# Kernel optimization log

Measured on AMD Instinct MI355X. Metric: run time of the kernel, lower is better.

Reference implementation:

```python
import jax, jax.numpy as jnp
import numpy as np

B, N, E, H = 2, 2048, 512, 8
D = E // H
SCALE_BASE = 512.0
EPS = 1e-6


def _xpos_tables(n, d):
    # XPOS (torchscale): per-dim scale ramp + standard sinusoidal freqs
    half = d // 2
    xscale = (np.arange(0, d, 2, dtype=np.float32) + 0.4 * d) / (1.4 * d)  # [half]
    min_pos = -(n // 2)
    power = (np.arange(min_pos, n + min_pos, dtype=np.float32) / SCALE_BASE)[:, None]
    scale = xscale[None, :] ** power                                       # [n, half]
    inv_freq = 1.0 / (10000.0 ** (np.arange(0, half, dtype=np.float32) / half))
    sinusoid = np.arange(n, dtype=np.float32)[:, None] * inv_freq[None, :]  # [n, half]
    return (jnp.asarray(np.sin(sinusoid), jnp.float32),
            jnp.asarray(np.cos(sinusoid), jnp.float32),
            jnp.asarray(scale, jnp.float32))


def _dup_interleave(m):
    # [n, half] -> [n, d], each column repeated twice interleaved
    return jnp.repeat(m, 2, axis=-1)


def _rotate_every_two(x):
    x1, x2 = x[..., ::2], x[..., 1::2]
    return jnp.stack((-x2, x1), axis=-1).reshape(x.shape)


def _apply_xpos(x, sin, cos, scale):
    s = _dup_interleave(sin * scale)  # [n, d]
    c = _dup_interleave(cos * scale)
    return x * c + _rotate_every_two(x) * s


def _decay_mask(n, dtype=jnp.float32):
    # gammas per head: 1 - exp(linspace(log(1/32), log(1/512), H))
    gammas = 1.0 - jnp.exp(jnp.linspace(np.log(1.0 / 32), np.log(1.0 / 512), H)).astype(dtype)
    pos = jnp.arange(n, dtype=dtype)
    dist = pos[:, None] - pos[None, :]                 # [n, s]
    dist_c = jnp.where(dist >= 0, dist, 0.0)
    return jnp.where(dist[None] >= 0, gammas[:, None, None] ** dist_c[None], 0.0)  # [h, n, s]


def _msr_forward(query, key, value, Wq, bq, Wk, bk, Wv, bv, Wg, bg, Wo, bo):
    b, n, e = query.shape
    q = (query @ Wq.T + bq).reshape(b, n, H, D).transpose(0, 2, 1, 3)  # [b,h,n,d]
    k = (key   @ Wk.T + bk).reshape(b, n, H, D).transpose(0, 2, 1, 3)
    v = (value @ Wv.T + bv).reshape(b, n, H, D).transpose(0, 2, 1, 3)

    sin, cos, scale = _xpos_tables(n, D)
    q = _apply_xpos(q, sin, cos, scale)
    k = _apply_xpos(k, sin, cos, 1.0 / scale)  # downscale=True

    k = k / jnp.asarray(np.sqrt(D), q.dtype)   # scale = head_dim ** 0.5
    mask = _decay_mask(n, q.dtype)             # [h,n,s]

    sim = jnp.einsum('bhnd,bhsd->bhns', q, k) * mask[None]
    ret = jnp.einsum('bhns,bhsd->bhnd', sim, v)  # [b,h,n,d]

    # GroupNorm(groups=H, channels=H, affine=False) on [(b n), h, d]:
    # normalize each (b, n, h) slice over its d elements
    mean = ret.mean(axis=-1, keepdims=True)
    var = ret.var(axis=-1, keepdims=True)
    ret = (ret - mean) / jnp.sqrt(var + EPS)

    ret = ret.transpose(0, 2, 1, 3).reshape(b, n, e)
    gate = jax.nn.silu(query @ Wg.T + bg)
    return (ret * gate) @ Wo.T + bo


def setup_inputs() -> dict:
    key = jax.random.key(0)
    ks = jax.random.split(key, 13)
    std = float(np.sqrt(2.0 / (E + E)))  # xavier_normal for square Linear
    mk = lambda k: jax.random.normal(k, (E, E), jnp.float32) * std
    return {
        'query': jax.random.normal(ks[0], (B, N, E), jnp.float32),
        'key':   jax.random.normal(ks[1], (B, N, E), jnp.float32),
        'value': jax.random.normal(ks[2], (B, N, E), jnp.float32),
        'Wq': mk(ks[3]), 'bq': jnp.zeros((E,), jnp.float32),
        'Wk': mk(ks[4]), 'bk': jnp.zeros((E,), jnp.float32),
        'Wv': mk(ks[5]), 'bv': jnp.zeros((E,), jnp.float32),
        'Wg': mk(ks[6]), 'bg': jnp.zeros((E,), jnp.float32),
        'Wo': mk(ks[7]), 'bo': jnp.zeros((E,), jnp.float32),
    }


def reference(query, key, value, Wq, bq, Wk, bk, Wv, bv, Wg, bg, Wo, bo):
    return _msr_forward(query, key, value, Wq, bq, Wk, bk, Wv, bv, Wg, bg, Wo, bo)
```

## Files before the change

kernel.cpp:

```cpp
#include <hip/hip_runtime.h>
#include <math.h>

#define Bc 2
#define Nc 2048
#define Ec 512
#define Hc 8
#define Dc 64
#define Mc 4096
#define NT 32
#define Cc 64

typedef short bf16x8 __attribute__((ext_vector_type(8)));
typedef float f32x4 __attribute__((ext_vector_type(4)));

#define GLOAD(g, l) __builtin_amdgcn_global_load_lds(                        \
    (const __attribute__((address_space(1))) unsigned*)(const void*)(g),     \
    (__attribute__((address_space(3))) unsigned*)(void*)(l), 16, 0, 0)

__device__ __forceinline__ unsigned short f2bf(float x) {
    union { float f; unsigned u; } v; v.f = x;
    unsigned r = v.u + 0x7fffu + ((v.u >> 16) & 1u);
    return (unsigned short)(r >> 16);
}
__device__ __forceinline__ float bf2f(unsigned short b) {
    union { float f; unsigned u; } v; v.u = ((unsigned)b) << 16;
    return v.f;
}

__device__ __forceinline__ float get_gamma(int h) {
    const float l0 = -3.4657359028f;
    const float l1 = -6.2383246250f;
    return 1.0f - expf(l0 + (l1 - l0) * ((float)h / 7.0f));
}

struct SplitArgs {
    const float* src[8];
    unsigned short* hi[8];
    unsigned short* lo[8];
    int n[8];
};

__global__ __launch_bounds__(256) void prep_kernel(SplitArgs a,
                                                   float* __restrict__ sinS,
                                                   float* __restrict__ cosS,
                                                   float* __restrict__ sinIS,
                                                   float* __restrict__ cosIS) {
    int y = blockIdx.y;
    if (y == 8) {
        int idx = blockIdx.x * 256 + threadIdx.x;
        if (idx >= Nc * 32) return;
        int n = idx >> 5;
        int i = idx & 31;
        float xscale = (2.0f * (float)i + 25.6f) / 89.6f;
        float power  = ((float)n - 1024.0f) / 512.0f;
        float scale  = powf(xscale, power);
        float inv_freq = powf(10000.0f, -(float)i / 32.0f);
        float ang = (float)n * inv_freq;
        float s = sinf(ang), c = cosf(ang);
        sinS[idx]  = s * scale;
        cosS[idx]  = c * scale;
        float rs = 1.0f / scale;
        sinIS[idx] = s * rs;
        cosIS[idx] = c * rs;
        return;
    }
    int i4 = (blockIdx.x * 256 + threadIdx.x) * 4;
    if (i4 >= a.n[y]) return;
    float4 v = *(const float4*)&a.src[y][i4];
    ushort4 h, l;
    h.x = f2bf(v.x); l.x = f2bf(v.x - bf2f(h.x));
    h.y = f2bf(v.y); l.y = f2bf(v.y - bf2f(h.y));
    h.z = f2bf(v.z); l.z = f2bf(v.z - bf2f(h.z));
    h.w = f2bf(v.w); l.w = f2bf(v.w - bf2f(h.w));
    *(ushort4*)&a.hi[y][i4] = h;
    *(ushort4*)&a.lo[y][i4] = l;
}

template<int TM, int TN>
__global__ __launch_bounds__(256) void mgemm_kernel(
    const unsigned short* __restrict__ Xq_h, const unsigned short* __restrict__ Xq_l,
    const unsigned short* __restrict__ Xk_h, const unsigned short* __restrict__ Xk_l,
    const unsigned short* __restrict__ Xv_h, const unsigned short* __restrict__ Xv_l,
    const unsigned short* __restrict__ Xr_h, const unsigned short* __restrict__ Xr_l,
    const unsigned short* __restrict__ Wq_h, const unsigned short* __restrict__ Wq_l,
    const unsigned short* __restrict__ Wk_h, const unsigned short* __restrict__ Wk_l,
    const unsigned short* __restrict__ Wv_h, const unsigned short* __restrict__ Wv_l,
    const unsigned short* __restrict__ Wg_h, const unsigned short* __restrict__ Wg_l,
    const unsigned short* __restrict__ Wo_h, const unsigned short* __restrict__ Wo_l,
    const float* __restrict__ bq, const float* __restrict__ bk, const float* __restrict__ bv,
    const float* __restrict__ bg, const float* __restrict__ bo,
    float* __restrict__ Qr, float* __restrict__ Kr, float* __restrict__ Vr,
    float* __restrict__ G, float* __restrict__ Out,
    const float* __restrict__ sinS, const float* __restrict__ cosS,
    const float* __restrict__ sinIS, const float* __restrict__ cosIS,
    int mode_base)
{
    constexpr int MI  = TM / 32;
    constexpr int NI  = TN / 32;
    constexpr int BUF = (TM + TN) * 64;
    constexpr int GL  = (TM / 64 + TN / 64) * 2;
    constexpr int AL  = TM * 32;
    constexpr int BHo = TM * 64;
    constexpr int BLo = TM * 64 + TN * 32;

    int mode = mode_base + blockIdx.z;
    const unsigned short *Xh, *Xl, *Wh, *Wl; const float* bias;
    switch (mode) {
        case 0:  Xh = Xq_h; Xl = Xq_l; Wh = Wq_h; Wl = Wq_l; bias = bq; break;
        case 1:  Xh = Xk_h; Xl = Xk_l; Wh = Wk_h; Wl = Wk_l; bias = bk; break;
        case 2:  Xh = Xv_h; Xl = Xv_l; Wh = Wv_h; Wl = Wv_l; bias = bv; break;
        case 3:  Xh = Xq_h; Xl = Xq_l; Wh = Wg_h; Wl = Wg_l; bias = bg; break;
        default: Xh = Xr_h; Xl = Xr_l; Wh = Wo_h; Wl = Wo_l; bias = bo; break;
    }

    __shared__ __align__(16) short lds[2 * BUF];

    int tid  = threadIdx.x;
    int lane = tid & 63;
    int w    = tid >> 6;
    int wr   = w >> 1, wc = w & 1;
    int row0 = blockIdx.x * TM, col0 = blockIdx.y * TN;
    int lrow = lane & 15, lslot = lane >> 4;

    f32x4 acc[MI][NI];
    #pragma unroll
    for (int i = 0; i < MI; ++i)
        #pragma unroll
        for (int j = 0; j < NI; ++j) acc[i][j] = {0.f, 0.f, 0.f, 0.f};

    int aoff[MI], boff[NI];
    #pragma unroll
    for (int mi = 0; mi < MI; ++mi) {
        int r = wr * (TM / 2) + mi * 16 + lrow;
        aoff[mi] = (r * 4 + (lslot ^ ((r >> 1) & 3))) * 8;
    }
    #pragma unroll
    for (int ni = 0; ni < NI; ++ni) {
        int r = wc * (TN / 2) + ni * 16 + lrow;
        boff[ni] = (r * 4 + (lslot ^ ((r >> 1) & 3))) * 8;
    }

    auto stage = [&](int buf, int k0) {
        short* l = &lds[buf * BUF];
        #pragma unroll
        for (int i = 0; i < TM / 64; ++i) {
            int q = i * 256 + tid;
            int r = q >> 2;
            int sp = (q & 3) ^ ((r >> 1) & 3);
            int base = (i * 256 + (w << 6)) * 8;
            size_t ga = (size_t)(row0 + r) * Ec + k0 + sp * 8;
            GLOAD(Xh + ga, &l[base]);
            GLOAD(Xl + ga, &l[AL + base]);
        }
        #pragma unroll
        for (int i = 0; i < TN / 64; ++i) {
            int q = i * 256 + tid;
            int r = q >> 2;
            int sp = (q & 3) ^ ((r >> 1) & 3);
            int base = (i * 256 + (w << 6)) * 8;
            size_t gb = (size_t)(col0 + r) * Ec + k0 + sp * 8;
            GLOAD(Wh + gb, &l[BHo + base]);
            GLOAD(Wl + gb, &l[BLo + base]);
        }
    };

    stage(0, 0);
    for (int t = 0; t < Ec / 32; ++t) {
        int cur = t & 1;
        if (t < Ec / 32 - 1) {
            stage(cur ^ 1, (t + 1) * 32);
            if constexpr (GL == 8) asm volatile("s_waitcnt vmcnt(8)" ::: "memory");
            else                   asm volatile("s_waitcnt vmcnt(4)" ::: "memory");
        } else {
            asm volatile("s_waitcnt vmcnt(0)" ::: "memory");
        }
        __builtin_amdgcn_s_barrier();
        __builtin_amdgcn_sched_barrier(0);

        const short* l = &lds[cur * BUF];
        bf16x8 ah[MI], al2[MI], bh[NI], bl[NI];
        #pragma unroll
        for (int mi = 0; mi < MI; ++mi) {
            ah[mi]  = *(const bf16x8*)&l[aoff[mi]];
            al2[mi] = *(const bf16x8*)&l[AL + aoff[mi]];
        }
        #pragma unroll
        for (int ni = 0; ni < NI; ++ni) {
            bh[ni] = *(const bf16x8*)&l[BHo + boff[ni]];
            bl[ni] = *(const bf16x8*)&l[BLo + boff[ni]];
        }
        #pragma unroll
        for (int mi = 0; mi < MI; ++mi)
            #pragma unroll
            for (int ni = 0; ni < NI; ++ni) {
                acc[mi][ni] = __builtin_amdgcn_mfma_f32_16x16x32_bf16(ah[mi],  bh[ni], acc[mi][ni], 0, 0, 0);
                acc[mi][ni] = __builtin_amdgcn_mfma_f32_16x16x32_bf16(ah[mi],  bl[ni], acc[mi][ni], 0, 0, 0);
                acc[mi][ni] = __builtin_amdgcn_mfma_f32_16x16x32_bf16(al2[mi], bh[ni], acc[mi][ni], 0, 0, 0);
            }
        asm volatile("s_waitcnt lgkmcnt(0)" ::: "memory");
        __builtin_amdgcn_sched_barrier(0);
        __builtin_amdgcn_s_barrier();
    }

    int quad = lane >> 4;
    #pragma unroll
    for (int mi = 0; mi < MI; ++mi) {
        #pragma unroll
        for (int reg = 0; reg < 4; ++reg) {
            int R  = row0 + wr * (TM / 2) + mi * 16 + quad * 4 + reg;
            int bb = R >> 11;
            int n  = R & 2047;
            #pragma unroll
            for (int ni = 0; ni < NI; ++ni) {
                int c = col0 + wc * (TN / 2) + ni * 16 + lrow;
                float x = acc[mi][ni][reg] + bias[c];
                if (mode <= 1) {
                    float p = __shfl_xor(x, 1, 64);
                    int h = c >> 6, d = c & 63, pr = d >> 1;
                    const float* st = (mode == 0) ? sinS : sinIS;
                    const float* ct = (mode == 0) ? cosS : cosIS;
                    float sv = st[n * 32 + pr], cv = ct[n * 32 + pr];
                    float y = (c & 1) ? fmaf(x, cv,  p * sv)
                                      : fmaf(x, cv, -p * sv);
                    if (mode == 1) y *= 0.125f;
                    float* dst = (mode == 0) ? Qr : Kr;
                    dst[(((size_t)(bb * Hc + h)) * Nc + n) * Dc + d] = y;
                } else if (mode == 2) {
                    int h = c >> 6, d = c & 63;
                    Vr[(((size_t)(bb * Hc + h)) * Nc + n) * Dc + d] = x;
                } else if (mode == 3) {
                    G[(size_t)R * Ec + c] = x / (1.0f + expf(-x));
                } else {
                    Out[(size_t)R * Ec + c] = x;
                }
            }
        }
    }
}

__global__ __launch_bounds__(256) void phaseA_kernel(const float* __restrict__ Kr,
                                                     const float* __restrict__ Vr,
                                                     float* __restrict__ L)
{
    int bh = blockIdx.x;
    int t  = blockIdx.y;
    float gamma = get_gamma(bh & 7);
    float lg = logf(gamma);

    __shared__ float Ks[64][68];
    __shared__ float Vs[64][68];

    int tid = threadIdx.x;
    const float* Kc = Kr + (size_t)(bh * Nc + t * Cc) * Dc;
    const float* Vc = Vr + (size_t)(bh * Nc + t * Cc) * Dc;

    #pragma unroll
    for (int i = 0; i < 4; ++i) {
        int f = tid + i * 256;
        int s = f >> 4;
        int d = (f & 15) << 2;
        float w = expf(lg * (float)(Cc - s));
        float4 kv = *(const float4*)&Kc[s * Dc + d];
        float4 ks = {kv.x * w, kv.y * w, kv.z * w, kv.w * w};
        *(float4*)&Ks[s][d] = ks;
        float4 vv = *(const float4*)&Vc[s * Dc + d];
        *(float4*)&Vs[s][d] = vv;
    }
    __syncthreads();

    int tx = tid & 15, ty = tid >> 4;
    float acc[4][4];
    #pragma unroll
    for (int i = 0; i < 4; ++i)
        #pragma unroll
        for (int j = 0; j < 4; ++j) acc[i][j] = 0.0f;

    for (int s = 0; s < 64; ++s) {
        float4 a = *(const float4*)&Ks[s][ty * 4];
        float4 b = *(const float4*)&Vs[s][tx * 4];
        float av[4] = {a.x, a.y, a.z, a.w};
        float bv[4] = {b.x, b.y, b.z, b.w};
        #pragma unroll
        for (int i = 0; i < 4; ++i)
            #pragma unroll
            for (int j = 0; j < 4; ++j)
                acc[i][j] = fmaf(av[i], bv[j], acc[i][j]);
    }

    float* Lp = L + (size_t)(bh * NT + t) * 4096;
    #pragma unroll
    for (int i = 0; i < 4; ++i) {
        float4 o = {acc[i][0], acc[i][1], acc[i][2], acc[i][3]};
        *(float4*)&Lp[(ty * 4 + i) * 64 + tx * 4] = o;
    }
}

__global__ __launch_bounds__(256) void scan_kernel(const float* __restrict__ L,
                                                   float* __restrict__ Sst)
{
    int bh = blockIdx.x;
    int part = blockIdx.y;
    int tid = threadIdx.x;
    float gamma = get_gamma(bh & 7);
    float g64 = expf(logf(gamma) * 64.0f);

    float4 s = {0.0f, 0.0f, 0.0f, 0.0f};
    size_t base = (size_t)bh * NT * 4096 + part * 1024 + tid * 4;
    const float* Lp = L + base;
    float* Sp = Sst + base;
    for (int t = 0; t < NT; ++t) {
        *(float4*)&Sp[(size_t)t * 4096] = s;
        float4 l = *(const float4*)&Lp[(size_t)t * 4096];
        s.x = s.x * g64 + l.x;
        s.y = s.y * g64 + l.y;
        s.z = s.z * g64 + l.z;
        s.w = s.w * g64 + l.w;
    }
}

__global__ __launch_bounds__(256) void phaseC_kernel(
    const float* __restrict__ Qr, const float* __restrict__ Kr, const float* __restrict__ Vr,
    const float* __restrict__ Sst, const float* __restrict__ G,
    unsigned short* __restrict__ retGh, unsigned short* __restrict__ retGl)
{
    int bh = blockIdx.x, t = blockIdx.y;
    int b = bh >> 3, h = bh & 7;
    float gamma = get_gamma(h);
    float lg = logf(gamma);

    __shared__ float QsT[64][68];
    __shared__ float KsT[64][68];
    __shared__ float Ss[64][68];

    int tid = threadIdx.x;
    const float* Qc = Qr + (size_t)(bh * Nc + t * Cc) * Dc;
    const float* Kc = Kr + (size_t)(bh * Nc + t * Cc) * Dc;
    const float* Sp = Sst + (size_t)(bh * NT + t) * 4096;

    #pragma unroll
    for (int i = 0; i < 4; ++i) {
        int f = tid + i * 256;
        int r = f >> 4;
        int d = (f & 15) << 2;
        float wq = expf(lg * (float)r);
        float4 q = *(const float4*)&Qc[r * Dc + d];
        QsT[d + 0][r] = q.x * wq; QsT[d + 1][r] = q.y * wq;
        QsT[d + 2][r] = q.z * wq; QsT[d + 3][r] = q.w * wq;
        float wk = expf(-lg * (float)r);
        float4 kk = *(const float4*)&Kc[r * Dc + d];
        KsT[d + 0][r] = kk.x * wk; KsT[d + 1][r] = kk.y * wk;
        KsT[d + 2][r] = kk.z * wk; KsT[d + 3][r] = kk.w * wk;
        float4 sv = *(const float4*)&Sp[r * 64 + d];
        *(float4*)&Ss[r][d] = sv;
    }
    __syncthreads();

    int tx = tid & 15, ty = tid >> 4;
    float accA[4][4], accO[4][4];
    #pragma unroll
    for (int i = 0; i < 4; ++i)
        #pragma unroll
        for (int j = 0; j < 4; ++j) { accA[i][j] = 0.0f; accO[i][j] = 0.0f; }

    for (int d = 0; d < 64; ++d) {
        float4 a  = *(const float4*)&QsT[d][ty * 4];
        float4 kb = *(const float4*)&KsT[d][tx * 4];
        float4 sb = *(const float4*)&Ss[d][tx * 4];
        float av[4] = {a.x, a.y, a.z, a.w};
        float kv[4] = {kb.x, kb.y, kb.z, kb.w};
        float sv[4] = {sb.x, sb.y, sb.z, sb.w};
        #pragma unroll
        for (int i = 0; i < 4; ++i)
            #pragma unroll
            for (int j = 0; j < 4; ++j) {
                accA[i][j] = fmaf(av[i], kv[j], accA[i][j]);
                accO[i][j] = fmaf(av[i], sv[j], accO[i][j]);
            }
    }
    __syncthreads();

    #pragma unroll
    for (int i = 0; i < 4; ++i) {
        int gi = ty * 4 + i;
        #pragma unroll
        for (int j = 0; j < 4; ++j) {
            int gj = tx * 4 + j;
            KsT[gj][gi] = (gj <= gi) ? accA[i][j] : 0.0f;
        }
    }
    const float* Vc = Vr + (size_t)(bh * Nc + t * Cc) * Dc;
    #pragma unroll
    for (int i = 0; i < 4; ++i) {
        int f = tid + i * 256;
        int r = f >> 4;
        int d = (f & 15) << 2;
        float4 vv = *(const float4*)&Vc[r * Dc + d];
        *(float4*)&QsT[r][d] = vv;
    }
    __syncthreads();

    for (int j = 0; j < 64; ++j) {
        float4 a = *(const float4*)&KsT[j][ty * 4];
        float4 v = *(const float4*)&QsT[j][tx * 4];
        float av[4] = {a.x, a.y, a.z, a.w};
        float vv[4] = {v.x, v.y, v.z, v.w};
        #pragma unroll
        for (int i = 0; i < 4; ++i)
            #pragma unroll
            for (int jj = 0; jj < 4; ++jj)
                accO[i][jj] = fmaf(av[i], vv[jj], accO[i][jj]);
    }

    #pragma unroll
    for (int i = 0; i < 4; ++i) {
        float sum = accO[i][0] + accO[i][1] + accO[i][2] + accO[i][3];
        float sq  = accO[i][0] * accO[i][0] + accO[i][1] * accO[i][1]
                  + accO[i][2] * accO[i][2] + accO[i][3] * accO[i][3];
        #pragma unroll
        for (int m = 1; m < 16; m <<= 1) {
            sum += __shfl_xor(sum, m, 64);
            sq  += __shfl_xor(sq,  m, 64);
        }
        float mean = sum * (1.0f / 64.0f);
        float var  = sq * (1.0f / 64.0f) - mean * mean;
        float rinv = rsqrtf(var + 1e-6f);
        #pragma unroll
        for (int jj = 0; jj < 4; ++jj)
            accO[i][jj] = (accO[i][jj] - mean) * rinv;
    }

    #pragma unroll
    for (int i = 0; i < 4; ++i) {
        int n = t * Cc + ty * 4 + i;
        size_t idx = ((size_t)b * Nc + n) * Ec + h * Dc + tx * 4;
        float4 g = *(const float4*)&G[idx];
        float o0 = accO[i][0] * g.x, o1 = accO[i][1] * g.y;
        float o2 = accO[i][2] * g.z, o3 = accO[i][3] * g.w;
        ushort4 hh, ll;
        hh.x = f2bf(o0); ll.x = f2bf(o0 - bf2f(hh.x));
        hh.y = f2bf(o1); ll.y = f2bf(o1 - bf2f(hh.y));
        hh.z = f2bf(o2); ll.z = f2bf(o2 - bf2f(hh.z));
        hh.w = f2bf(o3); ll.w = f2bf(o3 - bf2f(hh.w));
        *(ushort4*)&retGh[idx] = hh;
        *(ushort4*)&retGl[idx] = ll;
    }
}

extern "C" void kernel_launch(void* const* d_in, const int* in_sizes, int n_in,
                              void* d_out, int out_size, void* d_ws, size_t ws_size,
                              hipStream_t stream) {
    const float* query = (const float*)d_in[0];
    const float* key   = (const float*)d_in[1];
    const float* value = (const float*)d_in[2];
    const float* Wq = (const float*)d_in[3];
    const float* bq = (const float*)d_in[4];
    const float* Wk = (const float*)d_in[5];
    const float* bk = (const float*)d_in[6];
    const float* Wv = (const float*)d_in[7];
    const float* bv = (const float*)d_in[8];
    const float* Wg = (const float*)d_in[9];
    const float* bg = (const float*)d_in[10];
    const float* Wo = (const float*)d_in[11];
    const float* bo = (const float*)d_in[12];
    float* out = (float*)d_out;

    float* wsf = (float*)d_ws;
    const size_t SZ = (size_t)Bc * Nc * Ec;

    float* Qr = wsf;
    float* Kr = Qr + SZ;
    float* Vr = Kr + SZ;
    float* G  = Vr + SZ;

    unsigned short* Xq_h = (unsigned short*)(wsf + 4 * SZ);
    unsigned short* Xq_l = Xq_h + SZ;
    unsigned short* Xk_h = Xq_l + SZ;
    unsigned short* Xk_l = Xk_h + SZ;
    unsigned short* Xv_h = Xk_l + SZ;
    unsigned short* Xv_l = Xv_h + SZ;
    float* L   = wsf + 4 * SZ;
    float* Sst = wsf + 5 * SZ;
    unsigned short* retGh = (unsigned short*)(wsf + 6 * SZ);
    unsigned short* retGl = retGh + SZ;

    const size_t WSZ = (size_t)Ec * Ec;
    unsigned short* Wp = (unsigned short*)(wsf + 7 * SZ);
    unsigned short* Wq_h = Wp;            unsigned short* Wq_l = Wp + WSZ;
    unsigned short* Wk_h = Wp + 2 * WSZ;  unsigned short* Wk_l = Wp + 3 * WSZ;
    unsigned short* Wv_h = Wp + 4 * WSZ;  unsigned short* Wv_l = Wp + 5 * WSZ;
    unsigned short* Wg_h = Wp + 6 * WSZ;  unsigned short* Wg_l = Wp + 7 * WSZ;
    unsigned short* Wo_h = Wp + 8 * WSZ;  unsigned short* Wo_l = Wp + 9 * WSZ;

    float* tab = wsf + 7 * SZ + (10 * WSZ) / 2;
    float* sinS  = tab;
    float* cosS  = sinS + Nc * 32;
    float* sinIS = cosS + Nc * 32;
    float* cosIS = sinIS + Nc * 32;

    SplitArgs sa;
    sa.src[0] = query; sa.hi[0] = Xq_h; sa.lo[0] = Xq_l; sa.n[0] = (int)SZ;
    sa.src[1] = key;   sa.hi[1] = Xk_h; sa.lo[1] = Xk_l; sa.n[1] = (int)SZ;
    sa.src[2] = value; sa.hi[2] = Xv_h; sa.lo[2] = Xv_l; sa.n[2] = (int)SZ;
    sa.src[3] = Wq;    sa.hi[3] = Wq_h; sa.lo[3] = Wq_l; sa.n[3] = (int)WSZ;
    sa.src[4] = Wk;    sa.hi[4] = Wk_h; sa.lo[4] = Wk_l; sa.n[4] = (int)WSZ;
    sa.src[5] = Wv;    sa.hi[5] = Wv_h; sa.lo[5] = Wv_l; sa.n[5] = (int)WSZ;
    sa.src[6] = Wg;    sa.hi[6] = Wg_h; sa.lo[6] = Wg_l; sa.n[6] = (int)WSZ;
    sa.src[7] = Wo;    sa.hi[7] = Wo_h; sa.lo[7] = Wo_l; sa.n[7] = (int)WSZ;
    prep_kernel<<<dim3(2048, 9), dim3(256), 0, stream>>>(sa, sinS, cosS, sinIS, cosIS);

    mgemm_kernel<128, 128><<<dim3(Mc / 128, Ec / 128, 4), dim3(256), 0, stream>>>(
        Xq_h, Xq_l, Xk_h, Xk_l, Xv_h, Xv_l, retGh, retGl,
        Wq_h, Wq_l, Wk_h, Wk_l, Wv_h, Wv_l, Wg_h, Wg_l, Wo_h, Wo_l,
        bq, bk, bv, bg, bo, Qr, Kr, Vr, G, out,
        sinS, cosS, sinIS, cosIS, 0);

    phaseA_kernel<<<dim3(Bc * Hc, NT), dim3(256), 0, stream>>>(Kr, Vr, L);
    scan_kernel<<<dim3(Bc * Hc, 4), dim3(256), 0, stream>>>(L, Sst);
    phaseC_kernel<<<dim3(Bc * Hc, NT), dim3(256), 0, stream>>>(Qr, Kr, Vr, Sst, G, retGh, retGl);

    mgemm_kernel<64, 64><<<dim3(Mc / 64, Ec / 64, 1), dim3(256), 0, stream>>>(
        Xq_h, Xq_l, Xk_h, Xk_l, Xv_h, Xv_l, retGh, retGl,
        Wq_h, Wq_l, Wk_h, Wk_l, Wv_h, Wv_l, Wg_h, Wg_l, Wo_h, Wo_l,
        bq, bk, bv, bg, bo, Qr, Kr, Vr, G, out,
        sinS, cosS, sinIS, cosIS, 4);
}
```

Measured before the change: 186.9 us.

## Load GEMM weight fragments directly to registers and restructure epilogue tables

```diff
diff --git a/kernel.cpp b/kernel.cpp
--- a/kernel.cpp
+++ b/kernel.cpp
@@ -16,6 +16,8 @@
 #define GLOAD(g, l) __builtin_amdgcn_global_load_lds(                        \
     (const __attribute__((address_space(1))) unsigned*)(const void*)(g),     \
     (__attribute__((address_space(3))) unsigned*)(void*)(l), 16, 0, 0)
+
+#define VMCNT(n) asm volatile("s_waitcnt vmcnt(" #n ")" ::: "memory")
 
 __device__ __forceinline__ unsigned short f2bf(float x) {
     union { float f; unsigned u; } v; v.f = x;
@@ -49,19 +51,20 @@
     if (y == 8) {
         int idx = blockIdx.x * 256 + threadIdx.x;
         if (idx >= Nc * 32) return;
-        int n = idx >> 5;
-        int i = idx & 31;
+        int n = idx & 2047;
+        int i = idx >> 11;
         float xscale = (2.0f * (float)i + 25.6f) / 89.6f;
         float power  = ((float)n - 1024.0f) / 512.0f;
         float scale  = powf(xscale, power);
         float inv_freq = powf(10000.0f, -(float)i / 32.0f);
         float ang = (float)n * inv_freq;
         float s = sinf(ang), c = cosf(ang);
-        sinS[idx]  = s * scale;
-        cosS[idx]  = c * scale;
-        float rs = 1.0f / scale;
-        sinIS[idx] = s * rs;
-        cosIS[idx] = c * rs;
+        int o = i * 2048 + n;
+        sinS[o]  = s * scale;
+        cosS[o]  = c * scale;
+        float rs = 0.125f / scale;
+        sinIS[o] = s * rs;
+        cosIS[o] = c * rs;
         return;
     }
     int i4 = (blockIdx.x * 256 + threadIdx.x) * 4;
@@ -76,8 +79,8 @@
     *(ushort4*)&a.lo[y][i4] = l;
 }
 
-template<int TM, int TN>
-__global__ __launch_bounds__(256) void mgemm_kernel(
+template<int TM, int TN, int WR, int WC>
+__global__ __launch_bounds__(WR * WC * 64, 2) void mgemm_kernel(
     const unsigned short* __restrict__ Xq_h, const unsigned short* __restrict__ Xq_l,
     const unsigned short* __restrict__ Xk_h, const unsigned short* __restrict__ Xk_l,
     const unsigned short* __restrict__ Xv_h, const unsigned short* __restrict__ Xv_l,
@@ -95,13 +98,16 @@
     const float* __restrict__ sinIS, const float* __restrict__ cosIS,
     int mode_base)
 {
-    constexpr int MI  = TM / 32;
-    constexpr int NI  = TN / 32;
-    constexpr int BUF = (TM + TN) * 64;
-    constexpr int GL  = (TM / 64 + TN / 64) * 2;
-    constexpr int AL  = TM * 32;
-    constexpr int BHo = TM * 64;
-    constexpr int BLo = TM * 64 + TN * 32;
+    constexpr int THREADS = WR * WC * 64;
+    constexpr int MI  = TM / WR / 16;
+    constexpr int NI  = TN / WC / 16;
+    constexpr int SAh = TM * 4 / THREADS;
+    constexpr int BUF = TM * 64;
+    constexpr int ALo = TM * 32;
+    constexpr int XFULL = 2 * SAh + 4 * NI;
+    constexpr int XTAIL = 2 * NI;
+    static_assert(XFULL == 20 || XFULL == 10, "vmcnt literal");
+    static_assert(XTAIL == 8 || XTAIL == 4, "vmcnt literal");
 
     int mode = mode_base + blockIdx.z;
     const unsigned short *Xh, *Xl, *Wh, *Wl; const float* bias;
@@ -118,7 +124,7 @@
     int tid  = threadIdx.x;
     int lane = tid & 63;
     int w    = tid >> 6;
-    int wr   = w >> 1, wc = w & 1;
+    int wr   = w / WC, wc = w % WC;
     int row0 = blockIdx.x * TM, col0 = blockIdx.y * TN;
     int lrow = lane & 15, lslot = lane >> 4;
 
@@ -128,110 +134,142 @@
         #pragma unroll
         for (int j = 0; j < NI; ++j) acc[i][j] = {0.f, 0.f, 0.f, 0.f};
 
-    int aoff[MI], boff[NI];
+    int aoff[MI];
     #pragma unroll
     for (int mi = 0; mi < MI; ++mi) {
-        int r = wr * (TM / 2) + mi * 16 + lrow;
+        int r = wr * (TM / WR) + mi * 16 + lrow;
         aoff[mi] = (r * 4 + (lslot ^ ((r >> 1) & 3))) * 8;
     }
-    #pragma unroll
-    for (int ni = 0; ni < NI; ++ni) {
-        int r = wc * (TN / 2) + ni * 16 + lrow;
-        boff[ni] = (r * 4 + (lslot ^ ((r >> 1) & 3))) * 8;
-    }
+    size_t wbase[NI];
+    #pragma unroll
+    for (int ni = 0; ni < NI; ++ni)
+        wbase[ni] = (size_t)(col0 + wc * (TN / WC) + ni * 16 + lrow) * Ec + lslot * 8;
 
     auto stage = [&](int buf, int k0) {
         short* l = &lds[buf * BUF];
         #pragma unroll
-        for (int i = 0; i < TM / 64; ++i) {
-            int q = i * 256 + tid;
+        for (int i = 0; i < SAh; ++i) {
+            int q = i * THREADS + tid;
             int r = q >> 2;
             int sp = (q & 3) ^ ((r >> 1) & 3);
-            int base = (i * 256 + (w << 6)) * 8;
+            int base = (i * THREADS + (w << 6)) * 8;
             size_t ga = (size_t)(row0 + r) * Ec + k0 + sp * 8;
             GLOAD(Xh + ga, &l[base]);
-            GLOAD(Xl + ga, &l[AL + base]);
-        }
-        #pragma unroll
-        for (int i = 0; i < TN / 64; ++i) {
-            int q = i * 256 + tid;
-            int r = q >> 2;
-            int sp = (q & 3) ^ ((r >> 1) & 3);
-            int base = (i * 256 + (w << 6)) * 8;
-            size_t gb = (size_t)(col0 + r) * Ec + k0 + sp * 8;
-            GLOAD(Wh + gb, &l[BHo + base]);
-            GLOAD(Wl + gb, &l[BLo + base]);
+            GLOAD(Xl + ga, &l[ALo + base]);
         }
     };
 
-    stage(0, 0);
-    for (int t = 0; t < Ec / 32; ++t) {
-        int cur = t & 1;
-        if (t < Ec / 32 - 1) {
-            stage(cur ^ 1, (t + 1) * 32);
-            if constexpr (GL == 8) asm volatile("s_waitcnt vmcnt(8)" ::: "memory");
-            else                   asm volatile("s_waitcnt vmcnt(4)" ::: "memory");
-        } else {
-            asm volatile("s_waitcnt vmcnt(0)" ::: "memory");
-        }
-        __builtin_amdgcn_s_barrier();
-        __builtin_amdgcn_sched_barrier(0);
-
-        const short* l = &lds[cur * BUF];
-        bf16x8 ah[MI], al2[MI], bh[NI], bl[NI];
+    bf16x8 whA[NI], wlA[NI], whB[NI], wlB[NI];
+    auto loadW = [&](bf16x8* dh, bf16x8* dl, int k0) {
+        #pragma unroll
+        for (int ni = 0; ni < NI; ++ni) {
+            dh[ni] = *(const bf16x8*)(Wh + wbase[ni] + k0);
+            dl[ni] = *(const bf16x8*)(Wl + wbase[ni] + k0);
+        }
+    };
+    auto step = [&](int bufi, const bf16x8* wh, const bf16x8* wl) {
+        const short* l = &lds[bufi * BUF];
+        bf16x8 ah[MI], al[MI];
         #pragma unroll
         for (int mi = 0; mi < MI; ++mi) {
-            ah[mi]  = *(const bf16x8*)&l[aoff[mi]];
-            al2[mi] = *(const bf16x8*)&l[AL + aoff[mi]];
-        }
-        #pragma unroll
-        for (int ni = 0; ni < NI; ++ni) {
-            bh[ni] = *(const bf16x8*)&l[BHo + boff[ni]];
-            bl[ni] = *(const bf16x8*)&l[BLo + boff[ni]];
+            ah[mi] = *(const bf16x8*)&l[aoff[mi]];
+            al[mi] = *(const bf16x8*)&l[ALo + aoff[mi]];
         }
         #pragma unroll
         for (int mi = 0; mi < MI; ++mi)
             #pragma unroll
             for (int ni = 0; ni < NI; ++ni) {
-                acc[mi][ni] = __builtin_amdgcn_mfma_f32_16x16x32_bf16(ah[mi],  bh[ni], acc[mi][ni], 0, 0, 0);
-                acc[mi][ni] = __builtin_amdgcn_mfma_f32_16x16x32_bf16(ah[mi],  bl[ni], acc[mi][ni], 0, 0, 0);
-                acc[mi][ni] = __builtin_amdgcn_mfma_f32_16x16x32_bf16(al2[mi], bh[ni], acc[mi][ni], 0, 0, 0);
+                acc[mi][ni] = __builtin_amdgcn_mfma_f32_16x16x32_bf16(ah[mi], wh[ni], acc[mi][ni], 0, 0, 0);
+                acc[mi][ni] = __builtin_amdgcn_mfma_f32_16x16x32_bf16(ah[mi], wl[ni], acc[mi][ni], 0, 0, 0);
+                acc[mi][ni] = __builtin_amdgcn_mfma_f32_16x16x32_bf16(al[mi], wh[ni], acc[mi][ni], 0, 0, 0);
             }
         asm volatile("s_waitcnt lgkmcnt(0)" ::: "memory");
         __builtin_amdgcn_sched_barrier(0);
         __builtin_amdgcn_s_barrier();
-    }
-
-    int quad = lane >> 4;
-    #pragma unroll
-    for (int mi = 0; mi < MI; ++mi) {
-        #pragma unroll
-        for (int reg = 0; reg < 4; ++reg) {
-            int R  = row0 + wr * (TM / 2) + mi * 16 + quad * 4 + reg;
-            int bb = R >> 11;
-            int n  = R & 2047;
-            #pragma unroll
-            for (int ni = 0; ni < NI; ++ni) {
-                int c = col0 + wc * (TN / 2) + ni * 16 + lrow;
-                float x = acc[mi][ni][reg] + bias[c];
-                if (mode <= 1) {
+    };
+
+    stage(0, 0);
+    loadW(whA, wlA, 0);
+    for (int t = 0; t < Ec / 32; t += 2) {
+        stage(1, (t + 1) * 32);
+        loadW(whB, wlB, (t + 1) * 32);
+        if constexpr (XFULL == 20) VMCNT(20); else VMCNT(10);
+        __builtin_amdgcn_s_barrier();
+        __builtin_amdgcn_sched_barrier(0);
+        step(0, whA, wlA);
+        if (t + 2 < Ec / 32) {
+            stage(0, (t + 2) * 32);
+            loadW(whA, wlA, (t + 2) * 32);
+            if constexpr (XFULL == 20) VMCNT(20); else VMCNT(10);
+        } else {
+            if constexpr (XTAIL == 8) VMCNT(8); else VMCNT(4);
+        }
+        __builtin_amdgcn_s_barrier();
+        __builtin_amdgcn_sched_barrier(0);
+        step(1, whB, wlB);
+    }
+
+    int quad = lslot;
+    if (mode <= 1) {
+        const float* st = (mode == 0) ? sinS : sinIS;
+        const float* ct = (mode == 0) ? cosS : cosIS;
+        float* dst = (mode == 0) ? Qr : Kr;
+        #pragma unroll
+        for (int ni = 0; ni < NI; ++ni) {
+            int c = col0 + wc * (TN / WC) + ni * 16 + lrow;
+            int h = c >> 6, d = c & 63, pr = d >> 1;
+            float bi = bias[c];
+            #pragma unroll
+            for (int mi = 0; mi < MI; ++mi) {
+                int R0 = row0 + wr * (TM / WR) + mi * 16 + quad * 4;
+                int bb = R0 >> 11;
+                int n0 = R0 & 2047;
+                float4 sv4 = *(const float4*)&st[pr * 2048 + n0];
+                float4 cv4 = *(const float4*)&ct[pr * 2048 + n0];
+                float svv[4] = {sv4.x, sv4.y, sv4.z, sv4.w};
+                float cvv[4] = {cv4.x, cv4.y, cv4.z, cv4.w};
+                #pragma unroll
+                for (int reg = 0; reg < 4; ++reg) {
+                    float x = acc[mi][ni][reg] + bi;
                     float p = __shfl_xor(x, 1, 64);
-                    int h = c >> 6, d = c & 63, pr = d >> 1;
-                    const float* st = (mode == 0) ? sinS : sinIS;
-                    const float* ct = (mode == 0) ? cosS : cosIS;
-                    float sv = st[n * 32 + pr], cv = ct[n * 32 + pr];
-                    float y = (c & 1) ? fmaf(x, cv,  p * sv)
-                                      : fmaf(x, cv, -p * sv);
-                    if (mode == 1) y *= 0.125f;
-                    float* dst = (mode == 0) ? Qr : Kr;
-                    dst[(((size_t)(bb * Hc + h)) * Nc + n) * Dc + d] = y;
-                } else if (mode == 2) {
-                    int h = c >> 6, d = c & 63;
-                    Vr[(((size_t)(bb * Hc + h)) * Nc + n) * Dc + d] = x;
-                } else if (mode == 3) {
-                    G[(size_t)R * Ec + c] = x / (1.0f + expf(-x));
-                } else {
-                    Out[(size_t)R * Ec + c] = x;
+                    float y = (c & 1) ? fmaf(x, cvv[reg],  p * svv[reg])
+                                      : fmaf(x, cvv[reg], -p * svv[reg]);
+                    dst[(((size_t)(bb * Hc + h)) * Nc + n0 + reg) * Dc + d] = y;
+                }
+            }
+        }
+    } else if (mode == 2) {
+        #pragma unroll
+        for (int ni = 0; ni < NI; ++ni) {
+            int c = col0 + wc * (TN / WC) + ni * 16 + lrow;
+            int h = c >> 6, d = c & 63;
+            float bi = bias[c];
+            #pragma unroll
+            for (int mi = 0; mi < MI; ++mi) {
+                int R0 = row0 + wr * (TM / WR) + mi * 16 + quad * 4;
+                int bb = R0 >> 11;
+                int n0 = R0 & 2047;
+                #pragma unroll
+                for (int reg = 0; reg < 4; ++reg)
+                    Vr[(((size_t)(bb * Hc + h)) * Nc + n0 + reg) * Dc + d] =
+                        acc[mi][ni][reg] + bi;
+            }
+        }
+    } else {
+        #pragma unroll
+        for (int ni = 0; ni < NI; ++ni) {
+            int c = col0 + wc * (TN / WC) + ni * 16 + lrow;
+            float bi = bias[c];
+            #pragma unroll
+            for (int mi = 0; mi < MI; ++mi) {
+                int R0 = row0 + wr * (TM / WR) + mi * 16 + quad * 4;
+                #pragma unroll
+                for (int reg = 0; reg < 4; ++reg) {
+                    float x = acc[mi][ni][reg] + bi;
+                    if (mode == 3)
+                        G[(size_t)(R0 + reg) * Ec + c] = x / (1.0f + expf(-x));
+                    else
+                        Out[(size_t)(R0 + reg) * Ec + c] = x;
                 }
             }
         }
@@ -508,7 +546,7 @@
     sa.src[7] = Wo;    sa.hi[7] = Wo_h; sa.lo[7] = Wo_l; sa.n[7] = (int)WSZ;
     prep_kernel<<<dim3(2048, 9), dim3(256), 0, stream>>>(sa, sinS, cosS, sinIS, cosIS);
 
-    mgemm_kernel<128, 128><<<dim3(Mc / 128, Ec / 128, 4), dim3(256), 0, stream>>>(
+    mgemm_kernel<128, 128, 2, 2><<<dim3(Mc / 128, Ec / 128, 4), dim3(256), 0, stream>>>(
         Xq_h, Xq_l, Xk_h, Xk_l, Xv_h, Xv_l, retGh, retGl,
         Wq_h, Wq_l, Wk_h, Wk_l, Wv_h, Wv_l, Wg_h, Wg_l, Wo_h, Wo_l,
         bq, bk, bv, bg, bo, Qr, Kr, Vr, G, out,
@@ -518,7 +556,7 @@
     scan_kernel<<<dim3(Bc * Hc, 4), dim3(256), 0, stream>>>(L, Sst);
     phaseC_kernel<<<dim3(Bc * Hc, NT), dim3(256), 0, stream>>>(Qr, Kr, Vr, Sst, G, retGh, retGl);
 
-    mgemm_kernel<64, 64><<<dim3(Mc / 64, Ec / 64, 1), dim3(256), 0, stream>>>(
+    mgemm_kernel<128, 64, 4, 2><<<dim3(Mc / 128, Ec / 64, 1), dim3(512), 0, stream>>>(
         Xq_h, Xq_l, Xk_h, Xk_l, Xv_h, Xv_l, retGh, retGl,
         Wq_h, Wq_l, Wk_h, Wk_l, Wv_h, Wv_l, Wg_h, Wg_l, Wo_h, Wo_l,
         bq, bk, bv, bg, bo, Qr, Kr, Vr, G, out,
```

Result: slower. 201.1 us (+7.6%).
